# Kernel optimization log

Hardware: AMD Instinct MI355X
Metric: run time of the kernel (lower is better)

The kernel has to match this reference:

```python
import jax, jax.numpy as jnp
import numpy as np

N_NODES = 50000
N_EDGES = 800000
IN_C, HID_C, OUT_C = 128, 128, 64


def setup_inputs() -> dict:
    key = jax.random.key(0)
    k = jax.random.split(key, 8)
    x = jax.random.normal(k[0], (N_NODES, IN_C), dtype=jnp.float32)
    edge_index = jax.random.randint(k[1], (2, N_EDGES), 0, N_NODES, dtype=jnp.int64)
    edge_weight = jax.random.uniform(k[2], (N_EDGES,), dtype=jnp.float32)
    # GCNConv parameters (glorot-style scale)
    W1 = jax.random.normal(k[3], (IN_C, HID_C), dtype=jnp.float32) * (1.0 / np.sqrt(IN_C))
    b1 = jnp.zeros((HID_C,), dtype=jnp.float32)
    W2 = jax.random.normal(k[4], (HID_C, OUT_C), dtype=jnp.float32) * (1.0 / np.sqrt(HID_C))
    b2 = jnp.zeros((OUT_C,), dtype=jnp.float32)
    return {"x": x, "edge_index": edge_index, "edge_weight": edge_weight,
            "W1": W1, "b1": b1, "W2": W2, "b2": b2}


def _gcn_conv(x, src, dst, edge_weight, W, b, num_nodes):
    # GCNConv(normalize=False): out[i] = sum_{(j->i) in E} w_ji * (x[j] @ W) + b
    h = x @ W                                  # [N, C_out] dense GEMM first (cheaper than per-edge)
    msg = h[src]                               # [E, C_out] gather
    if edge_weight is not None:
        msg = msg * edge_weight[:, None]
    agg = jax.ops.segment_sum(msg, dst, num_segments=num_nodes)  # scatter-add
    return agg + b


def reference(x, edge_index, edge_weight, W1, b1, W2, b2):
    # Eval mode: F.dropout(training=False) is identity.
    src, dst = edge_index[0], edge_index[1]
    n = x.shape[0]
    h = _gcn_conv(x, src, dst, edge_weight, W1, b1, n)
    h = jax.nn.relu(h)
    out = _gcn_conv(h, src, dst, None, W2, b2, n)  # second conv: no edge_weight
    return out
```

## Files before the change

kernel.cpp:

```cpp
#include <hip/hip_runtime.h>
#include <hip/hip_fp8.h>

#define N_NODES 50000
#define N_EDGES 800000
#define IN_C    128
#define HID_C   128
#define OUT_C   64

#define EPB     4096
#define SC_BLOCKS 196
#define NBUCKET 196
#define CAP     6144
#define G1_BLOCKS 782

typedef unsigned int   uint32;
typedef unsigned short ushort16;
typedef unsigned char  uchar8;
typedef __attribute__((ext_vector_type(8))) short short8;
typedef __attribute__((ext_vector_type(4))) float f32x4;

__device__ __forceinline__ ushort16 f2bf(float f) {
    uint32 u = __float_as_uint(f);
    u += 0x7FFFu + ((u >> 16) & 1u);
    return (ushort16)(u >> 16);
}
__device__ __forceinline__ float bf_lo(uint32 h) { return __uint_as_float(h << 16); }
__device__ __forceinline__ float bf_hi(uint32 h) { return __uint_as_float(h & 0xFFFF0000u); }

__device__ __forceinline__ ushort16 f2h_bits(float f) {
    union { _Float16 h; ushort16 u; } cv;
    cv.h = (_Float16)f;
    return cv.u;
}
__device__ __forceinline__ float h_bits2f(uint32 bits) {
    union { ushort16 u; _Float16 h; } cv;
    cv.u = (ushort16)bits;
    return (float)cv.h;
}
__device__ __forceinline__ uchar8 f2fp8(float f) {
    __hip_fp8_e4m3 t(f);
    return *reinterpret_cast<unsigned char*>(&t);
}
__device__ __forceinline__ float fp82f(uchar8 b) {
    __hip_fp8_e4m3 t;
    *reinterpret_cast<unsigned char*>(&t) = b;
    return (float)t;
}

__global__ __launch_bounds__(256) void prep_w_kernel(const float* __restrict__ W1,
                                                     const float* __restrict__ W2,
                                                     ushort16* __restrict__ W1t,
                                                     ushort16* __restrict__ W2t,
                                                     int* __restrict__ cursorC) {
    if (blockIdx.x == 0 && threadIdx.x < NBUCKET) cursorC[threadIdx.x] = 0;
    int i = blockIdx.x * 256 + threadIdx.x;
    if (i < 128 * 128) {
        int n = i / 128, k = i % 128;
        W1t[i] = f2bf(W1[k * 128 + n]);
    }
    int j = i - 128 * 128;
    if (j >= 0 && j < 64 * 128) {
        int n = j / 128, k = j % 128;
        W2t[j] = f2bf(W2[k * 64 + n]);
    }
}

__global__ __launch_bounds__(256) void gemm1_scatter_kernel(const float* __restrict__ x,
                                                            const ushort16* __restrict__ W1t,
                                                            uchar8* __restrict__ H1,
                                                            const int* __restrict__ ei,
                                                            const float* __restrict__ ew,
                                                            int* __restrict__ cursorC,
                                                            uint32* __restrict__ key32,
                                                            ushort16* __restrict__ wH) {
    __shared__ char smem[52224];
    const int tid = threadIdx.x;

    if (blockIdx.x < SC_BLOCKS) {
        int* hist  = (int*)smem;
        int* lbase = (int*)(smem + 1024);
        int blk = blockIdx.x;
        hist[tid] = 0;
        __syncthreads();
        int base = blk * EPB;
#pragma unroll
        for (int k = 0; k < EPB / 256; k++) {
            int e = base + tid + k * 256;
            if (e < N_EDGES) atomicAdd(&hist[ei[N_EDGES + e] >> 8], 1);
        }
        __syncthreads();
        int n = hist[tid];
        lbase[tid] = n ? atomicAdd(&cursorC[tid], n) : 0;
        __syncthreads();
        hist[tid] = 0;
        __syncthreads();
#pragma unroll
        for (int k = 0; k < EPB / 256; k++) {
            int e = base + tid + k * 256;
            if (e < N_EDGES) {
                int dst = ei[N_EDGES + e];
                int src = ei[e];
                float w = ew[e];
                int b = dst >> 8;
                int r = atomicAdd(&hist[b], 1);
                int pos = lbase[b] + r;
                if (pos < CAP) {
                    int slot = b * CAP + pos;
                    key32[slot] = ((uint32)(dst & 255) << 16) | (uint32)src;
                    wH[slot]    = f2h_bits(w);
                }
            }
        }
        return;
    }

    typedef ushort16 row136[136];
    row136* As = (row136*)smem;
    row136* Ws = (row136*)(smem + 64 * 136 * 2);

    const int wave = tid >> 6;
    const int lane = tid & 63;
    const int quad = lane >> 4;
    const int m    = lane & 15;
    const int blockRow = (blockIdx.x - SC_BLOCKS) * 64;

#pragma unroll
    for (int p = 0; p < 8; p++) {
        int u = tid + 256 * p;
        int row = u / 16, c8 = u % 16;
        uint4 v = ((const uint4*)W1t)[u];
        *((uint4*)&Ws[row][c8 * 8]) = v;
    }
#pragma unroll
    for (int p = 0; p < 8; p++) {
        int u = tid + 256 * p;
        int row = u / 32, c4 = u % 32;
        int gr = blockRow + row; if (gr > N_NODES - 1) gr = N_NODES - 1;
        float4 v = ((const float4*)x)[gr * 32 + c4];
        ushort4 s;
        s.x = f2bf(v.x); s.y = f2bf(v.y); s.z = f2bf(v.z); s.w = f2bf(v.w);
        *((ushort4*)&As[row][c4 * 4]) = s;
    }
    __syncthreads();

    f32x4 acc[8];
#pragma unroll
    for (int nt = 0; nt < 8; nt++) acc[nt] = (f32x4){0.f, 0.f, 0.f, 0.f};

#pragma unroll
    for (int kc = 0; kc < 128; kc += 32) {
        short8 a = *((const short8*)&As[wave * 16 + m][kc + quad * 8]);
#pragma unroll
        for (int nt = 0; nt < 8; nt++) {
            short8 b = *((const short8*)&Ws[nt * 16 + m][kc + quad * 8]);
            acc[nt] = __builtin_amdgcn_mfma_f32_16x16x32_bf16(a, b, acc[nt], 0, 0, 0);
        }
    }

    __syncthreads();
    uchar8* c8lds = (uchar8*)&As[0][0];
#pragma unroll
    for (int nt = 0; nt < 8; nt++)
#pragma unroll
        for (int r = 0; r < 4; r++)
            c8lds[(wave * 16 + quad * 4 + r) * 128 + nt * 16 + m] = f2fp8(acc[nt][r]);
    __syncthreads();
#pragma unroll
    for (int p = 0; p < 2; p++) {
        int u = tid + 256 * p;
        int row = u / 8, c16 = u % 8;
        int gr = blockRow + row;
        if (gr < N_NODES)
            ((uint4*)H1)[gr * 8 + c16] = *((const uint4*)&c8lds[row * 128 + c16 * 16]);
    }
}

__global__ __launch_bounds__(1024) void csr_fine_kernel(const uint32* __restrict__ key32,
                                                        const ushort16* __restrict__ wH,
                                                        const int* __restrict__ cursorC,
                                                        int* __restrict__ rowStart,
                                                        int* __restrict__ rowEnd,
                                                        uint32* __restrict__ pairs) {
    __shared__ uint32   keys[CAP];
    __shared__ ushort16 ws[CAP];
    __shared__ int hist[256];
    __shared__ int scan[256];
    int b = blockIdx.x, t = threadIdx.x;
    int s = b * CAP;
    int len = cursorC[b];
    if (len > CAP) len = CAP;
    if (t < 256) hist[t] = 0;
    __syncthreads();
    for (int j = t; j < len; j += 1024) {
        uint32 kv = key32[s + j];
        keys[j] = kv;
        ws[j]   = wH[s + j];
        atomicAdd(&hist[kv >> 16], 1);
    }
    __syncthreads();
    if (t < 256) scan[t] = hist[t];
    __syncthreads();
    for (int off = 1; off < 256; off <<= 1) {
        int a = 0;
        if (t < 256 && t >= off) a = scan[t - off];
        __syncthreads();
        if (t < 256) scan[t] += a;
        __syncthreads();
    }
    if (t < 256) {
        int excl = scan[t] - hist[t];
        hist[t] = excl;
        int node = b * 256 + t;
        if (node < N_NODES) {
            rowStart[node] = s + excl;
            rowEnd[node]   = s + scan[t];
        }
    }
    __syncthreads();
    for (int j = t; j < len; j += 1024) {
        uint32 kv = keys[j];
        int r = atomicAdd(&hist[kv >> 16], 1);
        pairs[s + r] = (kv & 0xFFFFu) | ((uint32)ws[j] << 16);
    }
}

template<int NT, bool ABF16, bool OUTFP8>
__global__ __launch_bounds__(256) void mfma_gemm_kernel(const void* __restrict__ Aptr,
                                                        const ushort16* __restrict__ Wt,
                                                        void* __restrict__ Cout, int M) {
    constexpr int N = NT * 16;
    __shared__ ushort16 As[64][136];
    __shared__ ushort16 Ws[N][136];

    const int tid  = threadIdx.x;
    const int wave = tid >> 6;
    const int lane = tid & 63;
    const int quad = lane >> 4;
    const int m    = lane & 15;
    const int blockRow = blockIdx.x * 64;

#pragma unroll
    for (int p = 0; p < N * 16 / 256; p++) {
        int u = tid + 256 * p;
        int row = u / 16, c8 = u % 16;
        uint4 v = ((const uint4*)Wt)[u];
        *((uint4*)&Ws[row][c8 * 8]) = v;
    }
    if (ABF16) {
#pragma unroll
        for (int p = 0; p < 4; p++) {
            int u = tid + 256 * p;
            int row = u / 16, c8 = u % 16;
            int gr = blockRow + row; if (gr > M - 1) gr = M - 1;
            uint4 v = ((const uint4*)Aptr)[gr * 16 + c8];
            *((uint4*)&As[row][c8 * 8]) = v;
        }
    } else {
#pragma unroll
        for (int p = 0; p < 8; p++) {
            int u = tid + 256 * p;
            int row = u / 32, c4 = u % 32;
            int gr = blockRow + row; if (gr > M - 1) gr = M - 1;
            float4 v = ((const float4*)Aptr)[gr * 32 + c4];
            ushort4 s;
            s.x = f2bf(v.x); s.y = f2bf(v.y); s.z = f2bf(v.z); s.w = f2bf(v.w);
            *((ushort4*)&As[row][c4 * 4]) = s;
        }
    }
    __syncthreads();

    f32x4 acc[NT];
#pragma unroll
    for (int nt = 0; nt < NT; nt++) acc[nt] = (f32x4){0.f, 0.f, 0.f, 0.f};

#pragma unroll
    for (int kc = 0; kc < 128; kc += 32) {
        short8 a = *((const short8*)&As[wave * 16 + m][kc + quad * 8]);
#pragma unroll
        for (int nt = 0; nt < NT; nt++) {
            short8 b = *((const short8*)&Ws[nt * 16 + m][kc + quad * 8]);
            acc[nt] = __builtin_amdgcn_mfma_f32_16x16x32_bf16(a, b, acc[nt], 0, 0, 0);
        }
    }

    __syncthreads();
    if (OUTFP8) {
        uchar8* c8lds = (uchar8*)&As[0][0];
#pragma unroll
        for (int nt = 0; nt < NT; nt++)
#pragma unroll
            for (int r = 0; r < 4; r++)
                c8lds[(wave * 16 + quad * 4 + r) * N + nt * 16 + m] = f2fp8(acc[nt][r]);
        __syncthreads();
#pragma unroll
        for (int p = 0; p < 64 * N / 16 / 256; p++) {
            int u = tid + 256 * p;
            int row = u / (N / 16), c16 = u % (N / 16);
            int gr = blockRow + row;
            if (gr < M)
                ((uint4*)Cout)[gr * (N / 16) + c16] = *((const uint4*)&c8lds[row * N + c16 * 16]);
        }
    } else {
#pragma unroll
        for (int nt = 0; nt < NT; nt++)
#pragma unroll
            for (int r = 0; r < 4; r++)
                As[wave * 16 + quad * 4 + r][nt * 16 + m] = f2bf(acc[nt][r]);
        __syncthreads();
#pragma unroll
        for (int p = 0; p < 64 * N / 8 / 256; p++) {
            int u = tid + 256 * p;
            int row = u / (N / 8), c8 = u % (N / 8);
            int gr = blockRow + row;
            if (gr < M)
                ((uint4*)Cout)[gr * (N / 8) + c8] = *((const uint4*)&As[row][c8 * 8]);
        }
    }
}

__global__ __launch_bounds__(256) void agg1_kernel(const ushort16* __restrict__ H1,
                                                   const int* __restrict__ rowStart,
                                                   const int* __restrict__ rowEnd,
                                                   const uint32* __restrict__ pairs,
                                                   const float* __restrict__ b1,
                                                   uint32* __restrict__ A1) {
    int node = blockIdx.x * 4 + (threadIdx.x >> 6);
    int lane = threadIdx.x & 63;
    if (node >= N_NODES) return;
    int s = rowStart[node], e = rowEnd[node];
    float2 acc = ((const float2*)b1)[lane];
    int i = s;
    for (; i + 8 <= e; i += 8) {
        uint32 p[8];
        ushort16 h[8];
#pragma unroll
        for (int j = 0; j < 8; j++) p[j] = pairs[i + j];
#pragma unroll
        for (int j = 0; j < 8; j++) h[j] = H1[(p[j] & 0xFFFFu) * 64 + lane];
#pragma unroll
        for (int j = 0; j < 8; j++) {
            float w = h_bits2f(p[j] >> 16);
            acc.x += w * fp82f((uchar8)(h[j] & 0xFF));
            acc.y += w * fp82f((uchar8)(h[j] >> 8));
        }
    }
    for (; i < e; i++) {
        uint32 p = pairs[i];
        ushort16 h = H1[(p & 0xFFFFu) * 64 + lane];
        float  w = h_bits2f(p >> 16);
        acc.x += w * fp82f((uchar8)(h & 0xFF));
        acc.y += w * fp82f((uchar8)(h >> 8));
    }
    float rx = fmaxf(acc.x, 0.f), ry = fmaxf(acc.y, 0.f);
    A1[node * 64 + lane] = (uint32)f2bf(rx) | ((uint32)f2bf(ry) << 16);
}

__global__ __launch_bounds__(256) void agg2_kernel(const uchar8* __restrict__ H2,
                                                   const int* __restrict__ rowStart,
                                                   const int* __restrict__ rowEnd,
                                                   const uint32* __restrict__ pairs,
                                                   const float* __restrict__ b2,
                                                   float* __restrict__ out) {
    int node = blockIdx.x * 4 + (threadIdx.x >> 6);
    int lane = threadIdx.x & 63;
    if (node >= N_NODES) return;
    int s = rowStart[node], e = rowEnd[node];
    float acc = b2[lane];
    int i = s;
    for (; i + 8 <= e; i += 8) {
        uchar8 v[8];
#pragma unroll
        for (int j = 0; j < 8; j++) v[j] = H2[(pairs[i + j] & 0xFFFFu) * 64 + lane];
#pragma unroll
        for (int j = 0; j < 8; j++) acc += fp82f(v[j]);
    }
    for (; i < e; i++)
        acc += fp82f(H2[(pairs[i] & 0xFFFFu) * 64 + lane]);
    out[node * 64 + lane] = acc;
}

extern "C" void kernel_launch(void* const* d_in, const int* in_sizes, int n_in,
                              void* d_out, int out_size, void* d_ws, size_t ws_size,
                              hipStream_t stream) {
    const float* x  = (const float*)d_in[0];
    const int*   ei = (const int*)  d_in[1];
    const float* ew = (const float*)d_in[2];
    const float* W1 = (const float*)d_in[3];
    const float* b1 = (const float*)d_in[4];
    const float* W2 = (const float*)d_in[5];
    const float* b2 = (const float*)d_in[6];
    float* out = (float*)d_out;

    uint32* H1      = (uint32*)d_ws;
    uint32* A1      = H1 + (size_t)N_NODES * 32;
    uint32* H2      = A1 + (size_t)N_NODES * 64;
    uint32* pairs   = H2 + (size_t)N_NODES * 16;
    uint32* key32   = pairs + (size_t)NBUCKET * CAP;
    ushort16* wH    = (ushort16*)(key32 + (size_t)NBUCKET * CAP);
    ushort16* W1t   = wH + (size_t)NBUCKET * CAP + (((size_t)NBUCKET * CAP) & 1);
    ushort16* W2t   = W1t + 128 * 128;
    int* cursorC    = (int*)(W2t + 64 * 128);
    int* rowStart   = cursorC + ((NBUCKET + 1) & ~1);
    int* rowEnd     = rowStart + N_NODES;

    const int nodeBlocks = (N_NODES + 3) / 4;

    prep_w_kernel<<<96, 256, 0, stream>>>(W1, W2, W1t, W2t, cursorC);

    gemm1_scatter_kernel<<<SC_BLOCKS + G1_BLOCKS, 256, 0, stream>>>(
        x, W1t, (uchar8*)H1, ei, ew, cursorC, key32, wH);

    csr_fine_kernel<<<NBUCKET, 1024, 0, stream>>>(key32, wH, cursorC, rowStart, rowEnd, pairs);

    agg1_kernel<<<nodeBlocks, 256, 0, stream>>>((const ushort16*)H1, rowStart, rowEnd, pairs, b1, A1);

    mfma_gemm_kernel<4, true, true><<<G1_BLOCKS, 256, 0, stream>>>(A1, W2t, H2, N_NODES);

    agg2_kernel<<<nodeBlocks, 256, 0, stream>>>((const uchar8*)H2, rowStart, rowEnd, pairs, b2, out);
}
```

Baseline: 181.1 us.

## Split aggregation wave into four edge-parallel quarter-waves with wider gathers

```diff
diff --git a/kernel.cpp b/kernel.cpp
--- a/kernel.cpp
+++ b/kernel.cpp
@@ -13,9 +13,10 @@
 #define CAP     6144
 #define G1_BLOCKS 782
 
-typedef unsigned int   uint32;
-typedef unsigned short ushort16;
-typedef unsigned char  uchar8;
+typedef unsigned int       uint32;
+typedef unsigned short     ushort16;
+typedef unsigned char      uchar8;
+typedef unsigned long long u64;
 typedef __attribute__((ext_vector_type(8))) short short8;
 typedef __attribute__((ext_vector_type(4))) float f32x4;
 
@@ -24,9 +25,6 @@
     u += 0x7FFFu + ((u >> 16) & 1u);
     return (ushort16)(u >> 16);
 }
-__device__ __forceinline__ float bf_lo(uint32 h) { return __uint_as_float(h << 16); }
-__device__ __forceinline__ float bf_hi(uint32 h) { return __uint_as_float(h & 0xFFFF0000u); }
-
 __device__ __forceinline__ ushort16 f2h_bits(float f) {
     union { _Float16 h; ushort16 u; } cv;
     cv.h = (_Float16)f;
@@ -45,6 +43,18 @@
     __hip_fp8_e4m3 t;
     *reinterpret_cast<unsigned char*>(&t) = b;
     return (float)t;
+}
+__device__ __forceinline__ void fp8x4_wacc(uint32 v, float w, f32x4& a) {
+    a.x += w * fp82f((uchar8)(v & 0xFF));
+    a.y += w * fp82f((uchar8)((v >> 8) & 0xFF));
+    a.z += w * fp82f((uchar8)((v >> 16) & 0xFF));
+    a.w += w * fp82f((uchar8)(v >> 24));
+}
+__device__ __forceinline__ void fp8x4_acc(uint32 v, f32x4& a) {
+    a.x += fp82f((uchar8)(v & 0xFF));
+    a.y += fp82f((uchar8)((v >> 8) & 0xFF));
+    a.z += fp82f((uchar8)((v >> 16) & 0xFF));
+    a.w += fp82f((uchar8)(v >> 24));
 }
 
 __global__ __launch_bounds__(256) void prep_w_kernel(const float* __restrict__ W1,
@@ -71,8 +81,7 @@
                                                             const int* __restrict__ ei,
                                                             const float* __restrict__ ew,
                                                             int* __restrict__ cursorC,
-                                                            uint32* __restrict__ key32,
-                                                            ushort16* __restrict__ wH) {
+                                                            u64* __restrict__ ebuf) {
     __shared__ char smem[52224];
     const int tid = threadIdx.x;
 
@@ -104,11 +113,9 @@
                 int b = dst >> 8;
                 int r = atomicAdd(&hist[b], 1);
                 int pos = lbase[b] + r;
-                if (pos < CAP) {
-                    int slot = b * CAP + pos;
-                    key32[slot] = ((uint32)(dst & 255) << 16) | (uint32)src;
-                    wH[slot]    = f2h_bits(w);
-                }
+                if (pos < CAP)
+                    ebuf[(size_t)b * CAP + pos] =
+                        ((u64)f2h_bits(w) << 32) | ((uint32)(dst & 255) << 16) | (uint32)src;
             }
         }
         return;
@@ -175,8 +182,7 @@
     }
 }
 
-__global__ __launch_bounds__(1024) void csr_fine_kernel(const uint32* __restrict__ key32,
-                                                        const ushort16* __restrict__ wH,
+__global__ __launch_bounds__(1024) void csr_fine_kernel(const u64* __restrict__ ebuf,
                                                         const int* __restrict__ cursorC,
                                                         int* __restrict__ rowStart,
                                                         int* __restrict__ rowEnd,
@@ -192,10 +198,11 @@
     if (t < 256) hist[t] = 0;
     __syncthreads();
     for (int j = t; j < len; j += 1024) {
-        uint32 kv = key32[s + j];
-        keys[j] = kv;
-        ws[j]   = wH[s + j];
-        atomicAdd(&hist[kv >> 16], 1);
+        u64 kv = ebuf[s + j];
+        uint32 lo = (uint32)kv;
+        keys[j] = lo;
+        ws[j]   = (ushort16)(kv >> 32);
+        atomicAdd(&hist[lo >> 16], 1);
     }
     __syncthreads();
     if (t < 256) scan[t] = hist[t];
@@ -318,65 +325,89 @@
     }
 }
 
-__global__ __launch_bounds__(256) void agg1_kernel(const ushort16* __restrict__ H1,
+__global__ __launch_bounds__(256) void agg1_kernel(const uint2* __restrict__ H1,
                                                    const int* __restrict__ rowStart,
                                                    const int* __restrict__ rowEnd,
                                                    const uint32* __restrict__ pairs,
                                                    const float* __restrict__ b1,
-                                                   uint32* __restrict__ A1) {
+                                                   uint4* __restrict__ A1) {
     int node = blockIdx.x * 4 + (threadIdx.x >> 6);
     int lane = threadIdx.x & 63;
+    int q = lane >> 4, cl = lane & 15;
     if (node >= N_NODES) return;
     int s = rowStart[node], e = rowEnd[node];
-    float2 acc = ((const float2*)b1)[lane];
-    int i = s;
-    for (; i + 8 <= e; i += 8) {
-        uint32 p[8];
-        ushort16 h[8];
-#pragma unroll
-        for (int j = 0; j < 8; j++) p[j] = pairs[i + j];
-#pragma unroll
-        for (int j = 0; j < 8; j++) h[j] = H1[(p[j] & 0xFFFFu) * 64 + lane];
-#pragma unroll
-        for (int j = 0; j < 8; j++) {
-            float w = h_bits2f(p[j] >> 16);
-            acc.x += w * fp82f((uchar8)(h[j] & 0xFF));
-            acc.y += w * fp82f((uchar8)(h[j] >> 8));
-        }
-    }
-    for (; i < e; i++) {
+    f32x4 aA = (f32x4){0.f, 0.f, 0.f, 0.f};
+    f32x4 aB = (f32x4){0.f, 0.f, 0.f, 0.f};
+    int i = s + q;
+    for (; i + 4 < e; i += 8) {
+        uint32 p0 = pairs[i], p1 = pairs[i + 4];
+        uint2 h0 = H1[(p0 & 0xFFFFu) * 16 + cl];
+        uint2 h1 = H1[(p1 & 0xFFFFu) * 16 + cl];
+        float w0 = h_bits2f(p0 >> 16), w1 = h_bits2f(p1 >> 16);
+        fp8x4_wacc(h0.x, w0, aA); fp8x4_wacc(h0.y, w0, aB);
+        fp8x4_wacc(h1.x, w1, aA); fp8x4_wacc(h1.y, w1, aB);
+    }
+    for (; i < e; i += 4) {
         uint32 p = pairs[i];
-        ushort16 h = H1[(p & 0xFFFFu) * 64 + lane];
-        float  w = h_bits2f(p >> 16);
-        acc.x += w * fp82f((uchar8)(h & 0xFF));
-        acc.y += w * fp82f((uchar8)(h >> 8));
-    }
-    float rx = fmaxf(acc.x, 0.f), ry = fmaxf(acc.y, 0.f);
-    A1[node * 64 + lane] = (uint32)f2bf(rx) | ((uint32)f2bf(ry) << 16);
-}
-
-__global__ __launch_bounds__(256) void agg2_kernel(const uchar8* __restrict__ H2,
+        uint2 h = H1[(p & 0xFFFFu) * 16 + cl];
+        float w = h_bits2f(p >> 16);
+        fp8x4_wacc(h.x, w, aA); fp8x4_wacc(h.y, w, aB);
+    }
+#pragma unroll
+    for (int d = 16; d <= 32; d <<= 1) {
+        aA.x += __shfl_xor(aA.x, d); aA.y += __shfl_xor(aA.y, d);
+        aA.z += __shfl_xor(aA.z, d); aA.w += __shfl_xor(aA.w, d);
+        aB.x += __shfl_xor(aB.x, d); aB.y += __shfl_xor(aB.y, d);
+        aB.z += __shfl_xor(aB.z, d); aB.w += __shfl_xor(aB.w, d);
+    }
+    if (q == 0) {
+        float4 b0 = ((const float4*)b1)[cl * 2];
+        float4 b4 = ((const float4*)b1)[cl * 2 + 1];
+        uint4 r;
+        r.x = (uint32)f2bf(fmaxf(aA.x + b0.x, 0.f)) | ((uint32)f2bf(fmaxf(aA.y + b0.y, 0.f)) << 16);
+        r.y = (uint32)f2bf(fmaxf(aA.z + b0.z, 0.f)) | ((uint32)f2bf(fmaxf(aA.w + b0.w, 0.f)) << 16);
+        r.z = (uint32)f2bf(fmaxf(aB.x + b4.x, 0.f)) | ((uint32)f2bf(fmaxf(aB.y + b4.y, 0.f)) << 16);
+        r.w = (uint32)f2bf(fmaxf(aB.z + b4.z, 0.f)) | ((uint32)f2bf(fmaxf(aB.w + b4.w, 0.f)) << 16);
+        A1[node * 16 + cl] = r;
+    }
+}
+
+__global__ __launch_bounds__(256) void agg2_kernel(const uint32* __restrict__ H2,
                                                    const int* __restrict__ rowStart,
                                                    const int* __restrict__ rowEnd,
                                                    const uint32* __restrict__ pairs,
                                                    const float* __restrict__ b2,
-                                                   float* __restrict__ out) {
+                                                   float4* __restrict__ out) {
     int node = blockIdx.x * 4 + (threadIdx.x >> 6);
     int lane = threadIdx.x & 63;
+    int q = lane >> 4, cl = lane & 15;
     if (node >= N_NODES) return;
     int s = rowStart[node], e = rowEnd[node];
-    float acc = b2[lane];
-    int i = s;
-    for (; i + 8 <= e; i += 8) {
-        uchar8 v[8];
-#pragma unroll
-        for (int j = 0; j < 8; j++) v[j] = H2[(pairs[i + j] & 0xFFFFu) * 64 + lane];
-#pragma unroll
-        for (int j = 0; j < 8; j++) acc += fp82f(v[j]);
-    }
-    for (; i < e; i++)
-        acc += fp82f(H2[(pairs[i] & 0xFFFFu) * 64 + lane]);
-    out[node * 64 + lane] = acc;
+    f32x4 acc = (f32x4){0.f, 0.f, 0.f, 0.f};
+    int i = s + q;
+    for (; i + 4 < e; i += 8) {
+        uint32 p0 = pairs[i], p1 = pairs[i + 4];
+        uint32 v0 = H2[(p0 & 0xFFFFu) * 16 + cl];
+        uint32 v1 = H2[(p1 & 0xFFFFu) * 16 + cl];
+        fp8x4_acc(v0, acc);
+        fp8x4_acc(v1, acc);
+    }
+    for (; i < e; i += 4) {
+        uint32 v = H2[(pairs[i] & 0xFFFFu) * 16 + cl];
+        fp8x4_acc(v, acc);
+    }
+#pragma unroll
+    for (int d = 16; d <= 32; d <<= 1) {
+        acc.x += __shfl_xor(acc.x, d); acc.y += __shfl_xor(acc.y, d);
+        acc.z += __shfl_xor(acc.z, d); acc.w += __shfl_xor(acc.w, d);
+    }
+    if (q == 0) {
+        float4 bb = ((const float4*)b2)[cl];
+        float4 r;
+        r.x = acc.x + bb.x; r.y = acc.y + bb.y;
+        r.z = acc.z + bb.z; r.w = acc.w + bb.w;
+        out[node * 16 + cl] = r;
+    }
 }
 
 extern "C" void kernel_launch(void* const* d_in, const int* in_sizes, int n_in,
@@ -395,9 +426,8 @@
     uint32* A1      = H1 + (size_t)N_NODES * 32;
     uint32* H2      = A1 + (size_t)N_NODES * 64;
     uint32* pairs   = H2 + (size_t)N_NODES * 16;
-    uint32* key32   = pairs + (size_t)NBUCKET * CAP;
-    ushort16* wH    = (ushort16*)(key32 + (size_t)NBUCKET * CAP);
-    ushort16* W1t   = wH + (size_t)NBUCKET * CAP + (((size_t)NBUCKET * CAP) & 1);
+    u64* ebuf       = (u64*)(pairs + (size_t)NBUCKET * CAP);
+    ushort16* W1t   = (ushort16*)(ebuf + (size_t)NBUCKET * CAP);
     ushort16* W2t   = W1t + 128 * 128;
     int* cursorC    = (int*)(W2t + 64 * 128);
     int* rowStart   = cursorC + ((NBUCKET + 1) & ~1);
@@ -408,13 +438,13 @@
     prep_w_kernel<<<96, 256, 0, stream>>>(W1, W2, W1t, W2t, cursorC);
 
     gemm1_scatter_kernel<<<SC_BLOCKS + G1_BLOCKS, 256, 0, stream>>>(
-        x, W1t, (uchar8*)H1, ei, ew, cursorC, key32, wH);
-
-    csr_fine_kernel<<<NBUCKET, 1024, 0, stream>>>(key32, wH, cursorC, rowStart, rowEnd, pairs);
-
-    agg1_kernel<<<nodeBlocks, 256, 0, stream>>>((const ushort16*)H1, rowStart, rowEnd, pairs, b1, A1);
+        x, W1t, (uchar8*)H1, ei, ew, cursorC, ebuf);
+
+    csr_fine_kernel<<<NBUCKET, 1024, 0, stream>>>(ebuf, cursorC, rowStart, rowEnd, pairs);
+
+    agg1_kernel<<<nodeBlocks, 256, 0, stream>>>((const uint2*)H1, rowStart, rowEnd, pairs, b1, (uint4*)A1);
 
     mfma_gemm_kernel<4, true, true><<<G1_BLOCKS, 256, 0, stream>>>(A1, W2t, H2, N_NODES);
 
-    agg2_kernel<<<nodeBlocks, 256, 0, stream>>>((const uchar8*)H2, rowStart, rowEnd, pairs, b2, out);
-}
+    agg2_kernel<<<nodeBlocks, 256, 0, stream>>>((const uint32*)H2, rowStart, rowEnd, pairs, b2, (float4*)out);
+}
```

Result: faster. 166.7 us (-8.0%).
